# Kernel tuning notes

Hardware: AMD Instinct MI355X
Metric: run time of the kernel (lower is better)

The kernel has to match this reference:

```python
import jax, jax.numpy as jnp
import numpy as np

EPSILON = 1e-06

def setup_inputs() -> dict:
    key = jax.random.key(0)
    k1, k2, k3 = jax.random.split(key, 3)
    B, S, D = 4, 4096, 4096
    x = jax.random.normal(k1, (B, S, D), dtype=jnp.float32)
    residual = jax.random.normal(k2, (B, S, D), dtype=jnp.float32)
    gamma = jax.random.uniform(k3, (D,), dtype=jnp.float32)
    return {"x": x, "residual": residual, "gamma": gamma}

def reference(x, residual, gamma):
    # Pass 1: residual add + RMSNorm (row-wise over last dim)
    x_added = x + residual
    rstd = jax.lax.rsqrt(jnp.mean(jnp.square(x_added), axis=-1, keepdims=True) + EPSILON)
    output = x_added * rstd * gamma  # [B, S, D]
    # Pass 2: global abs-max dynamic int8 quantization
    max_val = jnp.max(jnp.abs(output))
    scale = max_val / 127.0
    q = jnp.clip(jnp.round(output / scale), -128, 127).astype(jnp.int8)
    return q
```

## Files before the change

### kernel.cpp

```cpp
#include <hip/hip_runtime.h>
#include <hip/hip_fp16.h>

#define DD 4096
#define NROWS 16384
#define EPS 1e-6f

typedef float  fx4 __attribute__((ext_vector_type(4)));
typedef int    ix4 __attribute__((ext_vector_type(4)));


__global__ __launch_bounds__(256) void pass1(
    const float* __restrict__ x, const float* __restrict__ res,
    const float* __restrict__ gamma, __half* __restrict__ yg,
    float* __restrict__ rstd, float* __restrict__ rowmax) {
  const int row = blockIdx.x;
  const int t = threadIdx.x;
  const fx4* x4 = (const fx4*)(x + (size_t)row * DD);
  const fx4* r4 = (const fx4*)(res + (size_t)row * DD);
  const fx4* g4 = (const fx4*)gamma;
  unsigned long long* yrow = (unsigned long long*)(yg + (size_t)row * DD);

  float ss = 0.f, mx = 0.f;
#pragma unroll
  for (int i = 0; i < 4; ++i) {
    const int idx = t + i * 256;
    fx4 xv = x4[idx], rv = r4[idx], gv = g4[idx];
    float y0 = xv.x + rv.x, y1 = xv.y + rv.y;
    float y2 = xv.z + rv.z, y3 = xv.w + rv.w;
    ss += y0 * y0 + y1 * y1 + y2 * y2 + y3 * y3;
    float p0 = y0 * gv.x, p1 = y1 * gv.y, p2 = y2 * gv.z, p3 = y3 * gv.w;
    mx = fmaxf(mx, fmaxf(fmaxf(fabsf(p0), fabsf(p1)),
                         fmaxf(fabsf(p2), fabsf(p3))));
    union { unsigned long long u; __half2 h2[2]; } pk;
    pk.h2[0] = __floats2half2_rn(p0, p1);
    pk.h2[1] = __floats2half2_rn(p2, p3);
    __builtin_nontemporal_store(pk.u, &yrow[idx]);
  }

#pragma unroll
  for (int off = 32; off > 0; off >>= 1) {
    ss += __shfl_down(ss, off, 64);
    mx = fmaxf(mx, __shfl_down(mx, off, 64));
  }
  __shared__ float s_ss[4], s_mx[4];
  const int wave = t >> 6, lane = t & 63;
  if (lane == 0) { s_ss[wave] = ss; s_mx[wave] = mx; }
  __syncthreads();
  if (t == 0) {
    float tss = s_ss[0] + s_ss[1] + s_ss[2] + s_ss[3];
    float tmx = fmaxf(fmaxf(s_mx[0], s_mx[1]), fmaxf(s_mx[2], s_mx[3]));
    float rs = rsqrtf(tss * (1.0f / DD) + EPS);
    rstd[row] = rs;
    rowmax[row] = tmx * rs;
  }
}

__global__ __launch_bounds__(1024) void reduce_gmax(
    const float* __restrict__ rowmax, float* __restrict__ gmax) {
  const int t = threadIdx.x;
  float m = 0.f;
#pragma unroll
  for (int i = 0; i < NROWS / 1024; ++i) m = fmaxf(m, rowmax[t + i * 1024]);
#pragma unroll
  for (int off = 32; off > 0; off >>= 1) m = fmaxf(m, __shfl_down(m, off, 64));
  __shared__ float s[16];
  if ((t & 63) == 0) s[t >> 6] = m;
  __syncthreads();
  if (t == 0) {
    float r = s[0];
#pragma unroll
    for (int i = 1; i < 16; ++i) r = fmaxf(r, s[i]);
    *gmax = r;
  }
}

__global__ __launch_bounds__(256) void pass2(
    const __half* __restrict__ yg, const float* __restrict__ rstd,
    const float* __restrict__ gmax, int* __restrict__ out) {
  const int row = blockIdx.x >> 1;
  const float c = rstd[row] * (127.0f / *gmax);
  const size_t base = ((size_t)blockIdx.x * 256 + threadIdx.x) * 8;
  union { ix4 v; __half h[8]; } u;
  u.v = *(const ix4*)(yg + base);
  ix4 q0, q1;
  q0.x = min(max(__float2int_rn(__half2float(u.h[0]) * c), -128), 127);
  q0.y = min(max(__float2int_rn(__half2float(u.h[1]) * c), -128), 127);
  q0.z = min(max(__float2int_rn(__half2float(u.h[2]) * c), -128), 127);
  q0.w = min(max(__float2int_rn(__half2float(u.h[3]) * c), -128), 127);
  q1.x = min(max(__float2int_rn(__half2float(u.h[4]) * c), -128), 127);
  q1.y = min(max(__float2int_rn(__half2float(u.h[5]) * c), -128), 127);
  q1.z = min(max(__float2int_rn(__half2float(u.h[6]) * c), -128), 127);
  q1.w = min(max(__float2int_rn(__half2float(u.h[7]) * c), -128), 127);
  *(ix4*)(out + base) = q0;
  *(ix4*)(out + base + 4) = q1;
}

__global__ __launch_bounds__(256) void pass1_nb(
    const float* __restrict__ x, const float* __restrict__ res,
    const float* __restrict__ gamma, float* __restrict__ rstd,
    float* __restrict__ rowmax) {
  const int row = blockIdx.x;
  const int t = threadIdx.x;
  const fx4* x4 = (const fx4*)(x + (size_t)row * DD);
  const fx4* r4 = (const fx4*)(res + (size_t)row * DD);
  const fx4* g4 = (const fx4*)gamma;
  float ss = 0.f, mx = 0.f;
#pragma unroll
  for (int i = 0; i < 4; ++i) {
    const int idx = t + i * 256;
    fx4 xv = x4[idx], rv = r4[idx], gv = g4[idx];
    float y0 = xv.x + rv.x, y1 = xv.y + rv.y;
    float y2 = xv.z + rv.z, y3 = xv.w + rv.w;
    ss += y0 * y0 + y1 * y1 + y2 * y2 + y3 * y3;
    mx = fmaxf(mx, fmaxf(fmaxf(fabsf(y0 * gv.x), fabsf(y1 * gv.y)),
                         fmaxf(fabsf(y2 * gv.z), fabsf(y3 * gv.w))));
  }
#pragma unroll
  for (int off = 32; off > 0; off >>= 1) {
    ss += __shfl_down(ss, off, 64);
    mx = fmaxf(mx, __shfl_down(mx, off, 64));
  }
  __shared__ float s_ss[4], s_mx[4];
  const int wave = t >> 6, lane = t & 63;
  if (lane == 0) { s_ss[wave] = ss; s_mx[wave] = mx; }
  __syncthreads();
  if (t == 0) {
    float tss = s_ss[0] + s_ss[1] + s_ss[2] + s_ss[3];
    float tmx = fmaxf(fmaxf(s_mx[0], s_mx[1]), fmaxf(s_mx[2], s_mx[3]));
    float rs = rsqrtf(tss * (1.0f / DD) + EPS);
    rstd[row] = rs;
    rowmax[row] = tmx * rs;
  }
}

__global__ __launch_bounds__(256) void pass2_nb(
    const float* __restrict__ x, const float* __restrict__ res,
    const float* __restrict__ gamma, const float* __restrict__ rstd,
    const float* __restrict__ gmax, int* __restrict__ out) {
  const int row = blockIdx.x;
  const int t = threadIdx.x;
  const float c = rstd[row] * (127.0f / *gmax);
  const fx4* x4 = (const fx4*)(x + (size_t)row * DD);
  const fx4* r4 = (const fx4*)(res + (size_t)row * DD);
  const fx4* g4 = (const fx4*)gamma;
  ix4* o4 = (ix4*)(out + (size_t)row * DD);
#pragma unroll
  for (int i = 0; i < 4; ++i) {
    const int idx = t + i * 256;
    fx4 xv = x4[idx], rv = r4[idx], gv = g4[idx];
    ix4 q;
    q.x = min(max(__float2int_rn((xv.x + rv.x) * gv.x * c), -128), 127);
    q.y = min(max(__float2int_rn((xv.y + rv.y) * gv.y * c), -128), 127);
    q.z = min(max(__float2int_rn((xv.z + rv.z) * gv.z * c), -128), 127);
    q.w = min(max(__float2int_rn((xv.w + rv.w) * gv.w * c), -128), 127);
    o4[idx] = q;
  }
}

extern "C" void kernel_launch(void* const* d_in, const int* in_sizes, int n_in,
                              void* d_out, int out_size, void* d_ws, size_t ws_size,
                              hipStream_t stream) {
  const float* x     = (const float*)d_in[0];
  const float* res   = (const float*)d_in[1];
  const float* gamma = (const float*)d_in[2];
  int* out = (int*)d_out;

  char* ws = (char*)d_ws;
  float* gmax   = (float*)ws;
  float* rowmax = (float*)(ws + 256);
  float* rstd   = (float*)(ws + 256 + 64 * 1024);
  const size_t yg_off = (size_t)1 << 20;
  const size_t need = yg_off + (size_t)NROWS * DD * 2;

  if (ws_size >= need) {
    __half* yg = (__half*)(ws + yg_off);
    pass1<<<NROWS, 256, 0, stream>>>(x, res, gamma, yg, rstd, rowmax);
    reduce_gmax<<<1, 1024, 0, stream>>>(rowmax, gmax);
    pass2<<<((size_t)NROWS * DD) / 2048, 256, 0, stream>>>(
        yg, rstd, gmax, out);
  } else {
    pass1_nb<<<NROWS, 256, 0, stream>>>(x, res, gamma, rstd, rowmax);
    reduce_gmax<<<1, 1024, 0, stream>>>(rowmax, gmax);
    pass2_nb<<<NROWS, 256, 0, stream>>>(x, res, gamma, rstd, gmax, out);
  }
}
```

Measured before the change: 206.6 us.

## Split pass1 into fp16 residual-sum stream and separate row-statistics kernel

Replaces the fused pass1 with two kernels. The first streams x+residual to an fp16 buffer, and the second rereads that buffer to compute the row sum of squares and the gamma-scaled max. pass2 now applies gamma itself, since the buffer holds the unscaled sum. This adds a full extra read of the 128MB fp16 buffer and an extra launch. It also computes the RMS statistics from fp16-rounded values, which may slightly change results.

```diff
diff --git a/kernel.cpp b/kernel.cpp
--- a/kernel.cpp
+++ b/kernel.cpp
@@ -9,34 +9,52 @@
 typedef int    ix4 __attribute__((ext_vector_type(4)));
 
 
-__global__ __launch_bounds__(256) void pass1(
+__global__ __launch_bounds__(256) void stream_y(
     const float* __restrict__ x, const float* __restrict__ res,
-    const float* __restrict__ gamma, __half* __restrict__ yg,
+    __half* __restrict__ yh) {
+  const size_t base4 = (size_t)blockIdx.x * 1024;
+  const fx4* x4 = (const fx4*)x + base4;
+  const fx4* r4 = (const fx4*)res + base4;
+  unsigned long long* y8 = (unsigned long long*)yh + base4;
+#pragma unroll
+  for (int i = 0; i < 4; ++i) {
+    const int idx = threadIdx.x + i * 256;
+    fx4 y = x4[idx] + r4[idx];
+    union { unsigned long long u; __half2 h2[2]; } c;
+    c.h2[0] = __floats2half2_rn(y.x, y.y);
+    c.h2[1] = __floats2half2_rn(y.z, y.w);
+    y8[idx] = c.u;
+  }
+}
+
+__global__ __launch_bounds__(256) void rowstat(
+    const __half* __restrict__ yh, const float* __restrict__ gamma,
     float* __restrict__ rstd, float* __restrict__ rowmax) {
   const int row = blockIdx.x;
   const int t = threadIdx.x;
-  const fx4* x4 = (const fx4*)(x + (size_t)row * DD);
-  const fx4* r4 = (const fx4*)(res + (size_t)row * DD);
-  const fx4* g4 = (const fx4*)gamma;
-  unsigned long long* yrow = (unsigned long long*)(yg + (size_t)row * DD);
+  const ix4* y16 = (const ix4*)(yh + (size_t)row * DD);
+  const fx4* g4 = (const fx4*)gamma;
 
   float ss = 0.f, mx = 0.f;
 #pragma unroll
-  for (int i = 0; i < 4; ++i) {
+  for (int i = 0; i < 2; ++i) {
     const int idx = t + i * 256;
-    fx4 xv = x4[idx], rv = r4[idx], gv = g4[idx];
-    float y0 = xv.x + rv.x, y1 = xv.y + rv.y;
-    float y2 = xv.z + rv.z, y3 = xv.w + rv.w;
-    ss += y0 * y0 + y1 * y1 + y2 * y2 + y3 * y3;
-    float p0 = y0 * gv.x, p1 = y1 * gv.y, p2 = y2 * gv.z, p3 = y3 * gv.w;
+    union { ix4 v; __half2 h2[4]; } u;
+    u.v = y16[idx];
+    fx4 ga = g4[idx * 2], gb = g4[idx * 2 + 1];
+    float2 f0 = __half22float2(u.h2[0]);
+    float2 f1 = __half22float2(u.h2[1]);
+    float2 f2 = __half22float2(u.h2[2]);
+    float2 f3 = __half22float2(u.h2[3]);
+    ss += f0.x * f0.x + f0.y * f0.y + f1.x * f1.x + f1.y * f1.y;
+    ss += f2.x * f2.x + f2.y * f2.y + f3.x * f3.x + f3.y * f3.y;
+    float p0 = f0.x * ga.x, p1 = f0.y * ga.y, p2 = f1.x * ga.z, p3 = f1.y * ga.w;
+    float p4 = f2.x * gb.x, p5 = f2.y * gb.y, p6 = f3.x * gb.z, p7 = f3.y * gb.w;
     mx = fmaxf(mx, fmaxf(fmaxf(fabsf(p0), fabsf(p1)),
                          fmaxf(fabsf(p2), fabsf(p3))));
-    union { unsigned long long u; __half2 h2[2]; } pk;
-    pk.h2[0] = __floats2half2_rn(p0, p1);
-    pk.h2[1] = __floats2half2_rn(p2, p3);
-    __builtin_nontemporal_store(pk.u, &yrow[idx]);
-  }
-
+    mx = fmaxf(mx, fmaxf(fmaxf(fabsf(p4), fabsf(p5)),
+                         fmaxf(fabsf(p6), fabsf(p7))));
+  }
 #pragma unroll
   for (int off = 32; off > 0; off >>= 1) {
     ss += __shfl_down(ss, off, 64);
@@ -75,24 +93,34 @@
 }
 
 __global__ __launch_bounds__(256) void pass2(
-    const __half* __restrict__ yg, const float* __restrict__ rstd,
-    const float* __restrict__ gmax, int* __restrict__ out) {
+    const __half* __restrict__ yh, const float* __restrict__ gamma,
+    const float* __restrict__ rstd, const float* __restrict__ gmax,
+    int* __restrict__ out) {
   const int row = blockIdx.x >> 1;
+  const int half = blockIdx.x & 1;
   const float c = rstd[row] * (127.0f / *gmax);
-  const size_t base = ((size_t)blockIdx.x * 256 + threadIdx.x) * 8;
-  union { ix4 v; __half h[8]; } u;
-  u.v = *(const ix4*)(yg + base);
+  const size_t ebase = (size_t)row * DD + half * 2048 + threadIdx.x * 8;
+  const int gidx = half * 512 + threadIdx.x * 2;
+  const fx4* g4 = (const fx4*)gamma;
+  fx4 ga = g4[gidx], gb = g4[gidx + 1];
+
+  union { ix4 v; __half2 h2[4]; } u;
+  u.v = *(const ix4*)(yh + ebase);
+  float2 f0 = __half22float2(u.h2[0]);
+  float2 f1 = __half22float2(u.h2[1]);
+  float2 f2 = __half22float2(u.h2[2]);
+  float2 f3 = __half22float2(u.h2[3]);
   ix4 q0, q1;
-  q0.x = min(max(__float2int_rn(__half2float(u.h[0]) * c), -128), 127);
-  q0.y = min(max(__float2int_rn(__half2float(u.h[1]) * c), -128), 127);
-  q0.z = min(max(__float2int_rn(__half2float(u.h[2]) * c), -128), 127);
-  q0.w = min(max(__float2int_rn(__half2float(u.h[3]) * c), -128), 127);
-  q1.x = min(max(__float2int_rn(__half2float(u.h[4]) * c), -128), 127);
-  q1.y = min(max(__float2int_rn(__half2float(u.h[5]) * c), -128), 127);
-  q1.z = min(max(__float2int_rn(__half2float(u.h[6]) * c), -128), 127);
-  q1.w = min(max(__float2int_rn(__half2float(u.h[7]) * c), -128), 127);
-  *(ix4*)(out + base) = q0;
-  *(ix4*)(out + base + 4) = q1;
+  q0.x = min(max(__float2int_rn(f0.x * ga.x * c), -128), 127);
+  q0.y = min(max(__float2int_rn(f0.y * ga.y * c), -128), 127);
+  q0.z = min(max(__float2int_rn(f1.x * ga.z * c), -128), 127);
+  q0.w = min(max(__float2int_rn(f1.y * ga.w * c), -128), 127);
+  q1.x = min(max(__float2int_rn(f2.x * gb.x * c), -128), 127);
+  q1.y = min(max(__float2int_rn(f2.y * gb.y * c), -128), 127);
+  q1.z = min(max(__float2int_rn(f3.x * gb.z * c), -128), 127);
+  q1.w = min(max(__float2int_rn(f3.y * gb.w * c), -128), 127);
+  *(ix4*)(out + ebase) = q0;
+  *(ix4*)(out + ebase + 4) = q1;
 }
 
 __global__ __launch_bounds__(256) void pass1_nb(
@@ -169,15 +197,15 @@
   float* gmax   = (float*)ws;
   float* rowmax = (float*)(ws + 256);
   float* rstd   = (float*)(ws + 256 + 64 * 1024);
-  const size_t yg_off = (size_t)1 << 20;
-  const size_t need = yg_off + (size_t)NROWS * DD * 2;
+  const size_t yh_off = (size_t)1 << 20;
+  const size_t need = yh_off + (size_t)NROWS * DD * 2;
 
   if (ws_size >= need) {
-    __half* yg = (__half*)(ws + yg_off);
-    pass1<<<NROWS, 256, 0, stream>>>(x, res, gamma, yg, rstd, rowmax);
+    __half* yh = (__half*)(ws + yh_off);
+    stream_y<<<NROWS, 256, 0, stream>>>(x, res, yh);
+    rowstat<<<NROWS, 256, 0, stream>>>(yh, gamma, rstd, rowmax);
     reduce_gmax<<<1, 1024, 0, stream>>>(rowmax, gmax);
-    pass2<<<((size_t)NROWS * DD) / 2048, 256, 0, stream>>>(
-        yg, rstd, gmax, out);
+    pass2<<<NROWS * 2, 256, 0, stream>>>(yh, gamma, rstd, gmax, out);
   } else {
     pass1_nb<<<NROWS, 256, 0, stream>>>(x, res, gamma, rstd, rowmax);
     reduce_gmax<<<1, 1024, 0, stream>>>(rowmax, gmax);
```

Result: slower. 243.9 us (+18.1%).

## Store per-row int8 intermediate instead of fp16 and requantize in pass2

Applied to the files above, without the earlier changes.

The first pass now computes the row sum of squares and the row abs-max. It then re-reads x, residual and gamma and writes the row quantized to int8, scaled by that row's own max. The second pass reads these packed bytes and rescales them by rowmax/gmax into the final int8 values. This halves the intermediate write and read traffic compared with fp16. In exchange it re-reads the inputs in pass1, which is cheap only if they are still in cache. Rounding twice can also shift results by one quantization step relative to the reference.

```diff
diff --git a/kernel.cpp b/kernel.cpp
--- a/kernel.cpp
+++ b/kernel.cpp
@@ -1,42 +1,34 @@
 #include <hip/hip_runtime.h>
-#include <hip/hip_fp16.h>
 
 #define DD 4096
 #define NROWS 16384
 #define EPS 1e-6f
 
-typedef float  fx4 __attribute__((ext_vector_type(4)));
-typedef int    ix4 __attribute__((ext_vector_type(4)));
+typedef float fx4 __attribute__((ext_vector_type(4)));
+typedef int   ix4 __attribute__((ext_vector_type(4)));
 
 
 __global__ __launch_bounds__(256) void pass1(
     const float* __restrict__ x, const float* __restrict__ res,
-    const float* __restrict__ gamma, __half* __restrict__ yg,
-    float* __restrict__ rstd, float* __restrict__ rowmax) {
+    const float* __restrict__ gamma, unsigned int* __restrict__ q8,
+    float* __restrict__ rowmax) {
   const int row = blockIdx.x;
   const int t = threadIdx.x;
   const fx4* x4 = (const fx4*)(x + (size_t)row * DD);
   const fx4* r4 = (const fx4*)(res + (size_t)row * DD);
   const fx4* g4 = (const fx4*)gamma;
-  unsigned long long* yrow = (unsigned long long*)(yg + (size_t)row * DD);
 
   float ss = 0.f, mx = 0.f;
 #pragma unroll
   for (int i = 0; i < 4; ++i) {
     const int idx = t + i * 256;
     fx4 xv = x4[idx], rv = r4[idx], gv = g4[idx];
-    float y0 = xv.x + rv.x, y1 = xv.y + rv.y;
-    float y2 = xv.z + rv.z, y3 = xv.w + rv.w;
-    ss += y0 * y0 + y1 * y1 + y2 * y2 + y3 * y3;
-    float p0 = y0 * gv.x, p1 = y1 * gv.y, p2 = y2 * gv.z, p3 = y3 * gv.w;
-    mx = fmaxf(mx, fmaxf(fmaxf(fabsf(p0), fabsf(p1)),
-                         fmaxf(fabsf(p2), fabsf(p3))));
-    union { unsigned long long u; __half2 h2[2]; } pk;
-    pk.h2[0] = __floats2half2_rn(p0, p1);
-    pk.h2[1] = __floats2half2_rn(p2, p3);
-    __builtin_nontemporal_store(pk.u, &yrow[idx]);
+    fx4 y = xv + rv;
+    ss += y.x * y.x + y.y * y.y + y.z * y.z + y.w * y.w;
+    fx4 p = y * gv;
+    mx = fmaxf(mx, fmaxf(fmaxf(fabsf(p.x), fabsf(p.y)),
+                         fmaxf(fabsf(p.z), fabsf(p.w))));
   }
-
 #pragma unroll
   for (int off = 32; off > 0; off >>= 1) {
     ss += __shfl_down(ss, off, 64);
@@ -46,12 +38,24 @@
   const int wave = t >> 6, lane = t & 63;
   if (lane == 0) { s_ss[wave] = ss; s_mx[wave] = mx; }
   __syncthreads();
-  if (t == 0) {
-    float tss = s_ss[0] + s_ss[1] + s_ss[2] + s_ss[3];
-    float tmx = fmaxf(fmaxf(s_mx[0], s_mx[1]), fmaxf(s_mx[2], s_mx[3]));
-    float rs = rsqrtf(tss * (1.0f / DD) + EPS);
-    rstd[row] = rs;
-    rowmax[row] = tmx * rs;
+  const float tss = s_ss[0] + s_ss[1] + s_ss[2] + s_ss[3];
+  const float tmx = fmaxf(fmaxf(s_mx[0], s_mx[1]), fmaxf(s_mx[2], s_mx[3]));
+  const float rs = rsqrtf(tss * (1.0f / DD) + EPS);
+  if (t == 0) rowmax[row] = tmx * rs;
+  const float inv = tmx > 0.f ? 127.0f / tmx : 0.f;
+
+  unsigned int* qrow = q8 + (size_t)row * (DD / 4);
+#pragma unroll
+  for (int i = 0; i < 4; ++i) {
+    const int idx = t + i * 256;
+    fx4 xv = x4[idx], rv = r4[idx], gv = g4[idx];
+    fx4 p = (xv + rv) * gv;
+    int a = min(max(__float2int_rn(p.x * inv), -127), 127);
+    int b = min(max(__float2int_rn(p.y * inv), -127), 127);
+    int c = min(max(__float2int_rn(p.z * inv), -127), 127);
+    int d = min(max(__float2int_rn(p.w * inv), -127), 127);
+    qrow[idx] = (unsigned int)(a & 255) | ((unsigned int)(b & 255) << 8) |
+                ((unsigned int)(c & 255) << 16) | ((unsigned int)(d & 255) << 24);
   }
 }
 
@@ -75,24 +79,23 @@
 }
 
 __global__ __launch_bounds__(256) void pass2(
-    const __half* __restrict__ yg, const float* __restrict__ rstd,
+    const unsigned int* __restrict__ q8, const float* __restrict__ rowmax,
     const float* __restrict__ gmax, int* __restrict__ out) {
-  const int row = blockIdx.x >> 1;
-  const float c = rstd[row] * (127.0f / *gmax);
-  const size_t base = ((size_t)blockIdx.x * 256 + threadIdx.x) * 8;
-  union { ix4 v; __half h[8]; } u;
-  u.v = *(const ix4*)(yg + base);
-  ix4 q0, q1;
-  q0.x = min(max(__float2int_rn(__half2float(u.h[0]) * c), -128), 127);
-  q0.y = min(max(__float2int_rn(__half2float(u.h[1]) * c), -128), 127);
-  q0.z = min(max(__float2int_rn(__half2float(u.h[2]) * c), -128), 127);
-  q0.w = min(max(__float2int_rn(__half2float(u.h[3]) * c), -128), 127);
-  q1.x = min(max(__float2int_rn(__half2float(u.h[4]) * c), -128), 127);
-  q1.y = min(max(__float2int_rn(__half2float(u.h[5]) * c), -128), 127);
-  q1.z = min(max(__float2int_rn(__half2float(u.h[6]) * c), -128), 127);
-  q1.w = min(max(__float2int_rn(__half2float(u.h[7]) * c), -128), 127);
-  *(ix4*)(out + base) = q0;
-  *(ix4*)(out + base + 4) = q1;
+  const int row = blockIdx.x;
+  const float c = rowmax[row] / *gmax;
+  const unsigned int* qrow = q8 + (size_t)row * (DD / 4);
+  ix4* orow = (ix4*)(out + (size_t)row * DD);
+#pragma unroll
+  for (int i = 0; i < 4; ++i) {
+    const int idx = threadIdx.x + i * 256;
+    const unsigned int w = qrow[idx];
+    ix4 q;
+    q.x = min(max(__float2int_rn((float)((int)(w << 24) >> 24) * c), -128), 127);
+    q.y = min(max(__float2int_rn((float)((int)(w << 16) >> 24) * c), -128), 127);
+    q.z = min(max(__float2int_rn((float)((int)(w << 8) >> 24) * c), -128), 127);
+    q.w = min(max(__float2int_rn((float)((int)w >> 24) * c), -128), 127);
+    orow[idx] = q;
+  }
 }
 
 __global__ __launch_bounds__(256) void pass1_nb(
@@ -109,11 +112,11 @@
   for (int i = 0; i < 4; ++i) {
     const int idx = t + i * 256;
     fx4 xv = x4[idx], rv = r4[idx], gv = g4[idx];
-    float y0 = xv.x + rv.x, y1 = xv.y + rv.y;
-    float y2 = xv.z + rv.z, y3 = xv.w + rv.w;
-    ss += y0 * y0 + y1 * y1 + y2 * y2 + y3 * y3;
-    mx = fmaxf(mx, fmaxf(fmaxf(fabsf(y0 * gv.x), fabsf(y1 * gv.y)),
-                         fmaxf(fabsf(y2 * gv.z), fabsf(y3 * gv.w))));
+    fx4 y = xv + rv;
+    ss += y.x * y.x + y.y * y.y + y.z * y.z + y.w * y.w;
+    fx4 p = y * gv;
+    mx = fmaxf(mx, fmaxf(fmaxf(fabsf(p.x), fabsf(p.y)),
+                         fmaxf(fabsf(p.z), fabsf(p.w))));
   }
 #pragma unroll
   for (int off = 32; off > 0; off >>= 1) {
@@ -169,15 +172,14 @@
   float* gmax   = (float*)ws;
   float* rowmax = (float*)(ws + 256);
   float* rstd   = (float*)(ws + 256 + 64 * 1024);
-  const size_t yg_off = (size_t)1 << 20;
-  const size_t need = yg_off + (size_t)NROWS * DD * 2;
+  const size_t q8_off = (size_t)1 << 20;
+  const size_t need = q8_off + (size_t)NROWS * DD;
 
   if (ws_size >= need) {
-    __half* yg = (__half*)(ws + yg_off);
-    pass1<<<NROWS, 256, 0, stream>>>(x, res, gamma, yg, rstd, rowmax);
+    unsigned int* q8 = (unsigned int*)(ws + q8_off);
+    pass1<<<NROWS, 256, 0, stream>>>(x, res, gamma, q8, rowmax);
     reduce_gmax<<<1, 1024, 0, stream>>>(rowmax, gmax);
-    pass2<<<((size_t)NROWS * DD) / 2048, 256, 0, stream>>>(
-        yg, rstd, gmax, out);
+    pass2<<<NROWS, 256, 0, stream>>>(q8, rowmax, gmax, out);
   } else {
     pass1_nb<<<NROWS, 256, 0, stream>>>(x, res, gamma, rstd, rowmax);
     reduce_gmax<<<1, 1024, 0, stream>>>(rowmax, gmax);
```

Result: faster. 196.4 us (-4.9%).
